# Performance work log

Measured on AMD Instinct MI355X. Metric: run time of the kernel, lower is better.

The kernel has to match this reference:

```python
import jax, jax.numpy as jnp
import numpy as np

H = 256
K = 16
EPS_LN = 1e-5


def setup_inputs() -> dict:
    key = jax.random.key(0)
    ks = jax.random.split(key, 24)
    B, N = 64, 256
    s = lambda *sh: 1.0 / np.sqrt(sh[0])
    inp = {
        "feat": jax.random.normal(ks[0], (B, N, H), jnp.float32),
        "centers": jax.random.normal(ks[1], (B, N, 3), jnp.float32),
        "text_global": jax.random.normal(ks[2], (B, H), jnp.float32),
        # geom_mlp: Linear(4,H) -> ReLU -> Linear(H,H) -> ReLU
        "w_geom1": jax.random.normal(ks[3], (4, H), jnp.float32) * s(4),
        "b_geom1": jnp.zeros((H,), jnp.float32),
        "w_geom2": jax.random.normal(ks[4], (H, H), jnp.float32) * s(H),
        "b_geom2": jnp.zeros((H,), jnp.float32),
        # text gate / bias projections
        "w_gate": jax.random.normal(ks[5], (H, H), jnp.float32) * s(H),
        "b_gate": jnp.zeros((H,), jnp.float32),
        "w_tbias": jax.random.normal(ks[6], (H, H), jnp.float32) * s(H),
        "b_tbias": jnp.zeros((H,), jnp.float32),
        # edge_mlp: Linear(H,H//2) -> ReLU -> Linear(H//2,1)
        "w_edge1": jax.random.normal(ks[7], (H, H // 2), jnp.float32) * s(H),
        "b_edge1": jnp.zeros((H // 2,), jnp.float32),
        "w_edge2": jax.random.normal(ks[8], (H // 2, 1), jnp.float32) * s(H // 2),
        "b_edge2": jnp.zeros((1,), jnp.float32),
        # msg_mlp: Linear(H,H) -> ReLU
        "w_msg": jax.random.normal(ks[9], (H, H), jnp.float32) * s(H),
        "b_msg": jnp.zeros((H,), jnp.float32),
        # out_proj: Linear(2H,H) -> ReLU
        "w_out": jax.random.normal(ks[10], (2 * H, H), jnp.float32) * s(2 * H),
        "b_out": jnp.zeros((H,), jnp.float32),
        # LayerNorm params
        "ln_gamma": jnp.ones((H,), jnp.float32),
        "ln_beta": jnp.zeros((H,), jnp.float32),
    }
    return inp


def _forward(feat, centers, text_global,
             w_geom1, b_geom1, w_geom2, b_geom2,
             w_gate, b_gate, w_tbias, b_tbias,
             w_edge1, b_edge1, w_edge2, b_edge2,
             w_msg, b_msg, w_out, b_out, ln_gamma, ln_beta):
    B, N, Hd = feat.shape
    k = min(K, N)
    # pairwise euclidean distances (B,N,N)
    sq = jnp.sum(centers * centers, axis=-1)  # (B,N)
    d2 = sq[:, :, None] + sq[:, None, :] - 2.0 * jnp.einsum('bnc,bmc->bnm', centers, centers)
    dist_matrix = jnp.sqrt(jnp.maximum(d2, 0.0))
    # k smallest -> top_k of negated distances (sorted ascending in distance)
    _, knn_idx = jax.lax.top_k(-dist_matrix, k)  # (B,N,k)
    idx_flat = knn_idx.reshape(B, N * k)
    feat_neigh = jnp.take_along_axis(feat, idx_flat[:, :, None], axis=1).reshape(B, N, k, Hd)
    centers_neigh = jnp.take_along_axis(centers, idx_flat[:, :, None], axis=1).reshape(B, N, k, 3)
    rel = centers_neigh - centers[:, :, None, :]  # (B,N,k,3)
    dist = jnp.linalg.norm(rel, axis=-1, keepdims=True) + 1e-6
    geom = jnp.concatenate([rel, jnp.log1p(dist)], axis=-1)  # (B,N,k,4)
    geom_emb = jax.nn.relu(jax.nn.relu(geom @ w_geom1 + b_geom1) @ w_geom2 + b_geom2)
    text_gate = jax.nn.sigmoid(text_global @ w_gate + b_gate)[:, None, None, :]
    text_bias = (text_global @ w_tbias + b_tbias)[:, None, None, :]
    geom_cond = geom_emb * text_gate + text_bias
    edge_feat = jnp.tanh(feat[:, :, None, :] + feat_neigh + geom_cond)  # (B,N,k,H)
    edge_logits = (jax.nn.relu(edge_feat @ w_edge1 + b_edge1) @ w_edge2 + b_edge2)[..., 0]
    edge_alpha = jax.nn.softmax(edge_logits, axis=-1)[..., None]  # (B,N,k,1)
    msg = jax.nn.relu(feat_neigh @ w_msg + b_msg)
    ctx = jnp.sum(edge_alpha * msg, axis=2)  # (B,N,H)
    out = jax.nn.relu(jnp.concatenate([feat, ctx], axis=-1) @ w_out + b_out)
    x = feat + out
    mu = jnp.mean(x, axis=-1, keepdims=True)
    var = jnp.mean((x - mu) ** 2, axis=-1, keepdims=True)
    return (x - mu) / jnp.sqrt(var + EPS_LN) * ln_gamma + ln_beta


def reference(feat, centers, text_global,
              w_geom1, b_geom1, w_geom2, b_geom2,
              w_gate, b_gate, w_tbias, b_tbias,
              w_edge1, b_edge1, w_edge2, b_edge2,
              w_msg, b_msg, w_out, b_out, ln_gamma, ln_beta):
    return _forward(feat, centers, text_global,
                    w_geom1, b_geom1, w_geom2, b_geom2,
                    w_gate, b_gate, w_tbias, b_tbias,
                    w_edge1, b_edge1, w_edge2, b_edge2,
                    w_msg, b_msg, w_out, b_out, ln_gamma, ln_beta)
```

## Files before the change

kernel.cpp:

```cpp
#include <hip/hip_runtime.h>

#define H 256
#define KNN 16
#define NPT 256
#define BB 64

typedef unsigned short u16;
typedef unsigned int u32;
typedef __attribute__((ext_vector_type(8))) short shortx8;
typedef __attribute__((ext_vector_type(4))) float floatx4;

__device__ __forceinline__ u16 f2b(float f) {
    u32 u = __float_as_uint(f);
    u32 r = (u + 0x7fffu + ((u >> 16) & 1u)) >> 16;
    return (u16)r;
}
__device__ __forceinline__ float b2f(u16 u) {
    return __uint_as_float(((u32)u) << 16);
}

__device__ __forceinline__ float fast_tanh(float x) {
    float e = __builtin_amdgcn_exp2f(x * 2.88539008177793f);
    return 1.0f - 2.0f * __builtin_amdgcn_rcpf(e + 1.0f);
}

__global__ __launch_bounds__(256) void prep_kernel(
    const float* __restrict__ feat,
    const float* __restrict__ w2, const float* __restrict__ we1,
    const float* __restrict__ wm, const float* __restrict__ wo,
    const float* __restrict__ w1, const float* __restrict__ b1,
    u16* __restrict__ w2t, u16* __restrict__ we1t,
    u16* __restrict__ wmt, u16* __restrict__ wot, u16* __restrict__ w1t,
    u16* __restrict__ featB) {
    int blk = blockIdx.x;
    if (blk < 1184) {
        int tid = blk * 256 + threadIdx.x;
        if (tid < 65536) {
            int n = tid >> 8, k = tid & 255;
            w2t[tid] = f2b(w2[k * 256 + n]);
        } else if (tid < 98304) {
            int t = tid - 65536;
            int n = t >> 8, k = t & 255;
            we1t[t] = f2b(we1[k * 128 + n]);
        } else if (tid < 163840) {
            int t = tid - 98304;
            int n = t >> 8, k = t & 255;
            wmt[t] = f2b(wm[k * 256 + n]);
        } else if (tid < 294912) {
            int t = tid - 163840;
            int n = t >> 9, k = t & 511;
            wot[t] = f2b(wo[k * 256 + n]);
        } else {
            int t = tid - 294912;
            int n = t >> 5, k = t & 31;
            float v = (k < 4) ? w1[k * 256 + n] : (k == 4 ? b1[n] : 0.0f);
            w1t[t] = f2b(v);
        }
        return;
    }
    int e = (blk - 1184) * 256 + threadIdx.x;
    float4 f = *(const float4*)&feat[(size_t)e * 4];
    uint2 st;
    st.x = (u32)f2b(f.x) | ((u32)f2b(f.y) << 16);
    st.y = (u32)f2b(f.z) | ((u32)f2b(f.w) << 16);
    *(uint2*)&featB[(size_t)e * 4] = st;
}

__global__ __launch_bounds__(256) void knn_kernel(const float* __restrict__ centers,
                                                  int* __restrict__ knn) {
    __shared__ float cx[NPT], cy[NPT], cz[NPT], sq[NPT];
    __shared__ float dl[4][64][17];
    __shared__ int il[4][64][17];
    int blk = blockIdx.x;
    int b = blk >> 2, n0 = (blk & 3) * 64;
    int h = threadIdx.x;
    int s = h >> 6, pt = h & 63;
    {
        const float* cb = centers + (size_t)b * NPT * 3;
        float x = cb[h * 3 + 0], y = cb[h * 3 + 1], z = cb[h * 3 + 2];
        cx[h] = x; cy[h] = y; cz[h] = z;
        sq[h] = x * x + y * y + z * z;
    }
    __syncthreads();
    int n = n0 + pt;
    float x = cx[n], y = cy[n], z = cz[n], sn = sq[n];
    float bd[KNN];
    int bi[KNN];
#pragma unroll
    for (int j = 0; j < KNN; j++) { bd[j] = 1e30f; bi[j] = 0x7fffffff; }
    for (int mm = 0; mm < 64; mm++) {
        int m = s * 64 + mm;
        float dot = x * cx[m] + y * cy[m] + z * cz[m];
        float d2 = (sn + sq[m]) - 2.0f * dot;
        float d = sqrtf(fmaxf(d2, 0.0f));
        if (d < bd[KNN - 1]) {
            bd[KNN - 1] = d; bi[KNN - 1] = m;
#pragma unroll
            for (int p = KNN - 1; p > 0; --p) {
                if (bd[p - 1] > bd[p]) {
                    float td = bd[p - 1]; bd[p - 1] = bd[p]; bd[p] = td;
                    int ti = bi[p - 1]; bi[p - 1] = bi[p]; bi[p] = ti;
                }
            }
        }
    }
#pragma unroll
    for (int j = 0; j < KNN; j++) { dl[s][pt][j] = bd[j]; il[s][pt][j] = bi[j]; }
    __syncthreads();
    if (s == 0) {
        float md[KNN];
        int mi[KNN];
#pragma unroll
        for (int j = 0; j < KNN; j++) { md[j] = dl[0][pt][j]; mi[j] = il[0][pt][j]; }
        for (int t = 1; t < 4; t++) {
            for (int j = 0; j < KNN; j++) {
                float d = dl[t][pt][j];
                int idx = il[t][pt][j];
                bool ins = (d < md[KNN - 1]) || (d == md[KNN - 1] && idx < mi[KNN - 1]);
                if (!ins) break;
                md[KNN - 1] = d; mi[KNN - 1] = idx;
#pragma unroll
                for (int p = KNN - 1; p > 0; --p) {
                    bool sw = (md[p - 1] > md[p]) ||
                              (md[p - 1] == md[p] && mi[p - 1] > mi[p]);
                    if (sw) {
                        float td = md[p - 1]; md[p - 1] = md[p]; md[p] = td;
                        int ti = mi[p - 1]; mi[p - 1] = mi[p]; mi[p] = ti;
                    }
                }
            }
        }
        int* kp = knn + (b * NPT + n0 + pt) * KNN;
#pragma unroll
        for (int j = 0; j < KNN; j++) kp[j] = mi[j];
    }
}

__global__ __launch_bounds__(512) void gate_kernel(const float* __restrict__ tg_g,
                                                   const float* __restrict__ wg,
                                                   const float* __restrict__ bg,
                                                   const float* __restrict__ wtb,
                                                   const float* __restrict__ btb,
                                                   float* __restrict__ gate,
                                                   float* __restrict__ tbias) {
    __shared__ float tg[H];
    int b = blockIdx.x, t = threadIdx.x;
    if (t < H) tg[t] = tg_g[b * H + t];
    __syncthreads();
    int h = t & 255;
    if (t < H) {
        float ag = bg[h];
#pragma unroll 4
        for (int i = 0; i < H; i++) ag += tg[i] * wg[i * H + h];
        gate[b * H + h] = 1.0f / (1.0f + expf(-ag));
    } else {
        float ab = btb[h];
#pragma unroll 4
        for (int i = 0; i < H; i++) ab += tg[i] * wtb[i * H + h];
        tbias[b * H + h] = ab;
    }
}

__global__ __launch_bounds__(256, 4) void msg_mfma(const u16* __restrict__ featB,
                                                   const u16* __restrict__ wmt,
                                                   const float* __restrict__ bm,
                                                   u16* __restrict__ MSGB) {
    __shared__ __attribute__((aligned(16))) u16 A[64][264];
    int p0 = blockIdx.x * 64, h = threadIdx.x;
    int w = h >> 6, lane = h & 63, quad = lane >> 4, lq = lane & 15;
#pragma unroll 8
    for (int row = 0; row < 64; row++)
        A[row][h] = featB[(size_t)(p0 + row) * H + h];
    __syncthreads();
    floatx4 acc[4][4];
#pragma unroll
    for (int rt = 0; rt < 4; rt++)
#pragma unroll
        for (int ct = 0; ct < 4; ct++) acc[rt][ct] = (floatx4){0, 0, 0, 0};
#pragma unroll 2
    for (int kt = 0; kt < 8; kt++) {
        shortx8 bf[4];
#pragma unroll
        for (int ct = 0; ct < 4; ct++)
            bf[ct] = *(const shortx8*)&wmt[(w * 64 + ct * 16 + lq) * 256 + kt * 32 + quad * 8];
#pragma unroll
        for (int rt = 0; rt < 4; rt++) {
            shortx8 a = *(const shortx8*)&A[rt * 16 + lq][kt * 32 + quad * 8];
#pragma unroll
            for (int ct = 0; ct < 4; ct++)
                acc[rt][ct] = __builtin_amdgcn_mfma_f32_16x16x32_bf16(a, bf[ct], acc[rt][ct], 0, 0, 0);
        }
    }
#pragma unroll
    for (int ct = 0; ct < 4; ct++) {
        int col = w * 64 + ct * 16 + lq;
        float bmc = bm[col];
#pragma unroll
        for (int rt = 0; rt < 4; rt++)
#pragma unroll
            for (int r = 0; r < 4; r++) {
                int row = rt * 16 + quad * 4 + r;
                MSGB[(size_t)(p0 + row) * H + col] = f2b(fmaxf(acc[rt][ct][r] + bmc, 0.0f));
            }
    }
}

__global__ __launch_bounds__(256, 4) void edge_mfma(
    const float* __restrict__ feat, const u16* __restrict__ featB,
    const float* __restrict__ centers,
    const u16* __restrict__ w1t,
    const u16* __restrict__ w2t, const float* __restrict__ b2v,
    const u16* __restrict__ we1t, const float* __restrict__ be1,
    const float* __restrict__ we2, const float* __restrict__ be2,
    const int* __restrict__ knn, const float* __restrict__ gateG,
    const float* __restrict__ tbiasG, const u16* __restrict__ MSGB,
    u16* __restrict__ ctxB) {
    __shared__ __attribute__((aligned(16))) u16 A[64][264];
    __shared__ float fnS[4][H];
    __shared__ __attribute__((aligned(16))) float geomS[64][4];
    __shared__ int nidxS[64];
    __shared__ float part[4][64];
    __shared__ float logitsS[64];
    __shared__ float alphaS[64];

    int bn0 = blockIdx.x * 4;
    int b = bn0 >> 8, n0 = bn0 & 255;
    int h = threadIdx.x;
    int w = h >> 6, lane = h & 63, quad = lane >> 4, lq = lane & 15;

    if (h < 64) nidxS[h] = knn[bn0 * KNN + h];
#pragma unroll
    for (int p = 0; p < 4; p++)
        fnS[p][h] = feat[(size_t)(bn0 + p) * H + h];
    if (h < 64) {
        int p = h >> 4;
        int m = nidxS[h];
        int n = n0 + p;
        const float* cb = centers + (size_t)b * NPT * 3;
        float rx = cb[m * 3 + 0] - cb[n * 3 + 0];
        float ry = cb[m * 3 + 1] - cb[n * 3 + 1];
        float rz = cb[m * 3 + 2] - cb[n * 3 + 2];
        float dist = sqrtf(rx * rx + ry * ry + rz * rz) + 1e-6f;
        geomS[h][0] = rx; geomS[h][1] = ry; geomS[h][2] = rz;
        geomS[h][3] = log1pf(dist);
    }
    __syncthreads();

    {
        shortx8 bw1[4];
#pragma unroll
        for (int ct = 0; ct < 4; ct++)
            bw1[ct] = *(const shortx8*)&w1t[(w * 64 + ct * 16 + lq) * 32 + quad * 8];
#pragma unroll
        for (int rt = 0; rt < 4; rt++) {
            shortx8 ag = {0, 0, 0, 0, 0, 0, 0, 0};
            if (quad == 0) {
                float4 g = *(const float4*)&geomS[rt * 16 + lq][0];
                ag[0] = (short)f2b(g.x);
                ag[1] = (short)f2b(g.y);
                ag[2] = (short)f2b(g.z);
                ag[3] = (short)f2b(g.w);
                ag[4] = (short)0x3F80;
            }
#pragma unroll
            for (int ct = 0; ct < 4; ct++) {
                floatx4 accg = __builtin_amdgcn_mfma_f32_16x16x32_bf16(
                    ag, bw1[ct], (floatx4){0, 0, 0, 0}, 0, 0, 0);
#pragma unroll
                for (int r = 0; r < 4; r++)
                    A[rt * 16 + quad * 4 + r][w * 64 + ct * 16 + lq] =
                        f2b(fmaxf(accg[r], 0.0f));
            }
        }
    }
    __syncthreads();

    floatx4 acc[4][4];
#pragma unroll
    for (int rt = 0; rt < 4; rt++)
#pragma unroll
        for (int ct = 0; ct < 4; ct++) acc[rt][ct] = (floatx4){0, 0, 0, 0};
#pragma unroll 2
    for (int kt = 0; kt < 8; kt++) {
        shortx8 bf[4];
#pragma unroll
        for (int ct = 0; ct < 4; ct++)
            bf[ct] = *(const shortx8*)&w2t[(w * 64 + ct * 16 + lq) * 256 + kt * 32 + quad * 8];
#pragma unroll
        for (int rt = 0; rt < 4; rt++) {
            shortx8 a = *(const shortx8*)&A[rt * 16 + lq][kt * 32 + quad * 8];
#pragma unroll
            for (int ct = 0; ct < 4; ct++)
                acc[rt][ct] = __builtin_amdgcn_mfma_f32_16x16x32_bf16(a, bf[ct], acc[rt][ct], 0, 0, 0);
        }
    }
    __syncthreads();

#pragma unroll
    for (int ct = 0; ct < 4; ct++) {
        int col = w * 64 + ct * 16 + lq;
        float b2c = b2v[col];
        float gc = gateG[b * H + col];
        float tc = tbiasG[b * H + col];
#pragma unroll
        for (int rt = 0; rt < 4; rt++) {
            float fnc = fnS[rt][col];
#pragma unroll
            for (int r = 0; r < 4; r++) {
                int row = rt * 16 + quad * 4 + r;
                float fb = b2f(featB[((size_t)b * NPT + nidxS[row]) * H + col]);
                float emb = fmaxf(acc[rt][ct][r] + b2c, 0.0f);
                float ef = fast_tanh(fnc + fb + emb * gc + tc);
                A[row][col] = f2b(ef);
            }
        }
    }
    __syncthreads();

    floatx4 acc2[4][2];
#pragma unroll
    for (int rt = 0; rt < 4; rt++)
#pragma unroll
        for (int c2 = 0; c2 < 2; c2++) acc2[rt][c2] = (floatx4){0, 0, 0, 0};
#pragma unroll 2
    for (int kt = 0; kt < 8; kt++) {
        shortx8 bf[2];
#pragma unroll
        for (int c2 = 0; c2 < 2; c2++)
            bf[c2] = *(const shortx8*)&we1t[(w * 32 + c2 * 16 + lq) * 256 + kt * 32 + quad * 8];
#pragma unroll
        for (int rt = 0; rt < 4; rt++) {
            shortx8 a = *(const shortx8*)&A[rt * 16 + lq][kt * 32 + quad * 8];
#pragma unroll
            for (int c2 = 0; c2 < 2; c2++)
                acc2[rt][c2] = __builtin_amdgcn_mfma_f32_16x16x32_bf16(a, bf[c2], acc2[rt][c2], 0, 0, 0);
        }
    }

    float pl[4][4];
#pragma unroll
    for (int rt = 0; rt < 4; rt++)
#pragma unroll
        for (int r = 0; r < 4; r++) pl[rt][r] = 0.0f;
#pragma unroll
    for (int c2 = 0; c2 < 2; c2++) {
        int col = w * 32 + c2 * 16 + lq;
        float be1c = be1[col], w2c = we2[col];
#pragma unroll
        for (int rt = 0; rt < 4; rt++)
#pragma unroll
            for (int r = 0; r < 4; r++)
                pl[rt][r] += fmaxf(acc2[rt][c2][r] + be1c, 0.0f) * w2c;
    }
#pragma unroll
    for (int d = 1; d < 16; d <<= 1)
#pragma unroll
        for (int rt = 0; rt < 4; rt++)
#pragma unroll
            for (int r = 0; r < 4; r++) pl[rt][r] += __shfl_xor(pl[rt][r], d, 16);
    if (lq == 0) {
#pragma unroll
        for (int rt = 0; rt < 4; rt++)
#pragma unroll
            for (int r = 0; r < 4; r++)
                part[w][rt * 16 + quad * 4 + r] = pl[rt][r];
    }
    __syncthreads();
    if (h < 64)
        logitsS[h] = part[0][h] + part[1][h] + part[2][h] + part[3][h] + be2[0];
    __syncthreads();
    if (h < 64) {
        int base = (h >> 4) * 16;
        float mx = -1e30f;
#pragma unroll
        for (int j = 0; j < KNN; j++) mx = fmaxf(mx, logitsS[base + j]);
        float sum = 0.0f;
#pragma unroll
        for (int j = 0; j < KNN; j++) sum += expf(logitsS[base + j] - mx);
        alphaS[h] = expf(logitsS[h] - mx) / sum;
    }
    __syncthreads();

    {
        int p = h >> 6, cg = (h & 63) * 4;
        float4 c = {0, 0, 0, 0};
#pragma unroll
        for (int j = 0; j < KNN; j++) {
            float al = alphaS[p * 16 + j];
            const u32* mp = (const u32*)&MSGB[((size_t)b * NPT + nidxS[p * 16 + j]) * H + cg];
            u32 m0 = mp[0], m1 = mp[1];
            c.x += al * __uint_as_float(m0 << 16);
            c.y += al * __uint_as_float(m0 & 0xFFFF0000u);
            c.z += al * __uint_as_float(m1 << 16);
            c.w += al * __uint_as_float(m1 & 0xFFFF0000u);
        }
        uint2 st;
        st.x = (u32)f2b(c.x) | ((u32)f2b(c.y) << 16);
        st.y = (u32)f2b(c.z) | ((u32)f2b(c.w) << 16);
        *(uint2*)&ctxB[(size_t)(bn0 + p) * H + cg] = st;
    }
}

__global__ __launch_bounds__(256, 4) void out_mfma(const float* __restrict__ feat,
                                                   const u16* __restrict__ featB,
                                                   const u16* __restrict__ ctxB,
                                                   const u16* __restrict__ wot,
                                                   const float* __restrict__ bo,
                                                   const float* __restrict__ gamma,
                                                   const float* __restrict__ beta,
                                                   float* __restrict__ out) {
    __shared__ __attribute__((aligned(16))) u16 A[32][520];
    __shared__ float redS[4][32], redS2[4][32];
    int p0 = blockIdx.x * 32, h = threadIdx.x;
    int w = h >> 6, lane = h & 63, quad = lane >> 4, lq = lane & 15;
#pragma unroll 8
    for (int row = 0; row < 32; row++) {
        A[row][h]       = featB[(size_t)(p0 + row) * H + h];
        A[row][256 + h] = ctxB[(size_t)(p0 + row) * H + h];
    }
    __syncthreads();
    floatx4 acc[2][4];
#pragma unroll
    for (int rt = 0; rt < 2; rt++)
#pragma unroll
        for (int ct = 0; ct < 4; ct++) acc[rt][ct] = (floatx4){0, 0, 0, 0};
#pragma unroll 2
    for (int kt = 0; kt < 16; kt++) {
        shortx8 bf[4];
#pragma unroll
        for (int ct = 0; ct < 4; ct++)
            bf[ct] = *(const shortx8*)&wot[(w * 64 + ct * 16 + lq) * 512 + kt * 32 + quad * 8];
#pragma unroll
        for (int rt = 0; rt < 2; rt++) {
            shortx8 a = *(const shortx8*)&A[rt * 16 + lq][kt * 32 + quad * 8];
#pragma unroll
            for (int ct = 0; ct < 4; ct++)
                acc[rt][ct] = __builtin_amdgcn_mfma_f32_16x16x32_bf16(a, bf[ct], acc[rt][ct], 0, 0, 0);
        }
    }
    float x[2][4][4];
    float sm[2][4], sq2[2][4];
#pragma unroll
    for (int rt = 0; rt < 2; rt++)
#pragma unroll
        for (int r = 0; r < 4; r++) { sm[rt][r] = 0.0f; sq2[rt][r] = 0.0f; }
#pragma unroll
    for (int rt = 0; rt < 2; rt++)
#pragma unroll
        for (int ct = 0; ct < 4; ct++) {
            int col = w * 64 + ct * 16 + lq;
            float boc = bo[col];
#pragma unroll
            for (int r = 0; r < 4; r++) {
                int row = rt * 16 + quad * 4 + r;
                float xx = feat[(size_t)(p0 + row) * H + col] +
                           fmaxf(acc[rt][ct][r] + boc, 0.0f);
                x[rt][ct][r] = xx;
                sm[rt][r] += xx;
                sq2[rt][r] += xx * xx;
            }
        }
#pragma unroll
    for (int d = 1; d < 16; d <<= 1)
#pragma unroll
        for (int rt = 0; rt < 2; rt++)
#pragma unroll
            for (int r = 0; r < 4; r++) {
                sm[rt][r] += __shfl_xor(sm[rt][r], d, 16);
                sq2[rt][r] += __shfl_xor(sq2[rt][r], d, 16);
            }
    if (lq == 0) {
#pragma unroll
        for (int rt = 0; rt < 2; rt++)
#pragma unroll
            for (int r = 0; r < 4; r++) {
                redS[w][rt * 16 + quad * 4 + r] = sm[rt][r];
                redS2[w][rt * 16 + quad * 4 + r] = sq2[rt][r];
            }
    }
    __syncthreads();
#pragma unroll
    for (int rt = 0; rt < 2; rt++)
#pragma unroll
        for (int r = 0; r < 4; r++) {
            int row = rt * 16 + quad * 4 + r;
            float s1 = redS[0][row] + redS[1][row] + redS[2][row] + redS[3][row];
            float s2 = redS2[0][row] + redS2[1][row] + redS2[2][row] + redS2[3][row];
            float mu = s1 * (1.0f / H);
            float var = s2 * (1.0f / H) - mu * mu;
            float inv = rsqrtf(fmaxf(var, 0.0f) + 1e-5f);
#pragma unroll
            for (int ct = 0; ct < 4; ct++) {
                int col = w * 64 + ct * 16 + lq;
                out[(size_t)(p0 + row) * H + col] =
                    (x[rt][ct][r] - mu) * inv * gamma[col] + beta[col];
            }
        }
}

extern "C" void kernel_launch(void* const* d_in, const int* in_sizes, int n_in,
                              void* d_out, int out_size, void* d_ws, size_t ws_size,
                              hipStream_t stream) {
    const float* feat    = (const float*)d_in[0];
    const float* centers = (const float*)d_in[1];
    const float* textg   = (const float*)d_in[2];
    const float* w1      = (const float*)d_in[3];
    const float* b1      = (const float*)d_in[4];
    const float* w2      = (const float*)d_in[5];
    const float* b2      = (const float*)d_in[6];
    const float* wg      = (const float*)d_in[7];
    const float* bg      = (const float*)d_in[8];
    const float* wtb     = (const float*)d_in[9];
    const float* btb     = (const float*)d_in[10];
    const float* we1     = (const float*)d_in[11];
    const float* be1     = (const float*)d_in[12];
    const float* we2     = (const float*)d_in[13];
    const float* be2     = (const float*)d_in[14];
    const float* wm      = (const float*)d_in[15];
    const float* bm      = (const float*)d_in[16];
    const float* wo      = (const float*)d_in[17];
    const float* bo      = (const float*)d_in[18];
    const float* gamma   = (const float*)d_in[19];
    const float* beta    = (const float*)d_in[20];

    char* ws = (char*)d_ws;
    size_t off = 0;
    int* knn     = (int*)(ws + off);   off += (size_t)BB * NPT * KNN * 4;
    float* gate  = (float*)(ws + off); off += (size_t)BB * H * 4;
    float* tbias = (float*)(ws + off); off += (size_t)BB * H * 4;
    u16* MSGB    = (u16*)(ws + off);   off += (size_t)BB * NPT * H * 2;
    u16* ctxB    = (u16*)(ws + off);   off += (size_t)BB * NPT * H * 2;
    u16* featB   = (u16*)(ws + off);   off += (size_t)BB * NPT * H * 2;
    u16* w2t     = (u16*)(ws + off);   off += (size_t)256 * 256 * 2;
    u16* we1t    = (u16*)(ws + off);   off += (size_t)128 * 256 * 2;
    u16* wmt     = (u16*)(ws + off);   off += (size_t)256 * 256 * 2;
    u16* wot     = (u16*)(ws + off);   off += (size_t)256 * 512 * 2;
    u16* w1t     = (u16*)(ws + off);   off += (size_t)256 * 32 * 2;

    prep_kernel<<<5280, 256, 0, stream>>>(feat, w2, we1, wm, wo, w1, b1,
                                          w2t, we1t, wmt, wot, w1t, featB);
    knn_kernel<<<256, 256, 0, stream>>>(centers, knn);
    gate_kernel<<<BB, 512, 0, stream>>>(textg, wg, bg, wtb, btb, gate, tbias);
    msg_mfma<<<BB * NPT / 64, 256, 0, stream>>>(featB, wmt, bm, MSGB);
    edge_mfma<<<BB * NPT / 4, 256, 0, stream>>>(feat, featB, centers, w1t, w2t, b2,
                                                we1t, be1, we2, be2, knn, gate, tbias,
                                                MSGB, ctxB);
    out_mfma<<<BB * NPT / 32, 256, 0, stream>>>(feat, featB, ctxB, wot, bo,
                                                gamma, beta, (float*)d_out);
}
```

Before: 347.3 us.

## Fuse output projection and LayerNorm into edge kernel, drop ctx buffer

Folds the out_proj GEMM, residual add and LayerNorm into the tail of edge_mfma. The 4 points' ctx and feat rows are staged in the existing shared A tile instead of writing ctxB to global and relaunching. This removes one kernel launch and the ctxB round trip through memory. In exchange each block runs a 16-row MFMA tile with only 4 valid rows, so 3/4 of the MFMA work is wasted. Each block also re-reads the full 256KB wot weight, which adds a lot of L2 traffic.

```diff
diff --git a/kernel.cpp b/kernel.cpp
--- a/kernel.cpp
+++ b/kernel.cpp
@@ -214,7 +214,9 @@
     const float* __restrict__ we2, const float* __restrict__ be2,
     const int* __restrict__ knn, const float* __restrict__ gateG,
     const float* __restrict__ tbiasG, const u16* __restrict__ MSGB,
-    u16* __restrict__ ctxB) {
+    const u16* __restrict__ wot, const float* __restrict__ bo,
+    const float* __restrict__ gamma, const float* __restrict__ beta,
+    float* __restrict__ out) {
     __shared__ __attribute__((aligned(16))) u16 A[64][264];
     __shared__ float fnS[4][H];
     __shared__ __attribute__((aligned(16))) float geomS[64][4];
@@ -381,6 +383,7 @@
     }
     __syncthreads();
 
+    u16* A2 = &A[0][0];
     {
         int p = h >> 6, cg = (h & 63) * 4;
         float4 c = {0, 0, 0, 0};
@@ -397,105 +400,73 @@
         uint2 st;
         st.x = (u32)f2b(c.x) | ((u32)f2b(c.y) << 16);
         st.y = (u32)f2b(c.z) | ((u32)f2b(c.w) << 16);
-        *(uint2*)&ctxB[(size_t)(bn0 + p) * H + cg] = st;
-    }
-}
-
-__global__ __launch_bounds__(256, 4) void out_mfma(const float* __restrict__ feat,
-                                                   const u16* __restrict__ featB,
-                                                   const u16* __restrict__ ctxB,
-                                                   const u16* __restrict__ wot,
-                                                   const float* __restrict__ bo,
-                                                   const float* __restrict__ gamma,
-                                                   const float* __restrict__ beta,
-                                                   float* __restrict__ out) {
-    __shared__ __attribute__((aligned(16))) u16 A[32][520];
-    __shared__ float redS[4][32], redS2[4][32];
-    int p0 = blockIdx.x * 32, h = threadIdx.x;
-    int w = h >> 6, lane = h & 63, quad = lane >> 4, lq = lane & 15;
-#pragma unroll 8
-    for (int row = 0; row < 32; row++) {
-        A[row][h]       = featB[(size_t)(p0 + row) * H + h];
-        A[row][256 + h] = ctxB[(size_t)(p0 + row) * H + h];
-    }
-    __syncthreads();
-    floatx4 acc[2][4];
-#pragma unroll
-    for (int rt = 0; rt < 2; rt++)
-#pragma unroll
-        for (int ct = 0; ct < 4; ct++) acc[rt][ct] = (floatx4){0, 0, 0, 0};
-#pragma unroll 2
+        *(uint2*)&A2[p * 520 + 256 + cg] = st;
+        uint2 fb2 = *(const uint2*)&featB[(size_t)(bn0 + p) * H + cg];
+        *(uint2*)&A2[p * 520 + cg] = fb2;
+    }
+    __syncthreads();
+
+    floatx4 acc3[4];
+#pragma unroll
+    for (int ct = 0; ct < 4; ct++) acc3[ct] = (floatx4){0, 0, 0, 0};
+#pragma unroll 4
     for (int kt = 0; kt < 16; kt++) {
-        shortx8 bf[4];
-#pragma unroll
-        for (int ct = 0; ct < 4; ct++)
-            bf[ct] = *(const shortx8*)&wot[(w * 64 + ct * 16 + lq) * 512 + kt * 32 + quad * 8];
-#pragma unroll
-        for (int rt = 0; rt < 2; rt++) {
-            shortx8 a = *(const shortx8*)&A[rt * 16 + lq][kt * 32 + quad * 8];
-#pragma unroll
-            for (int ct = 0; ct < 4; ct++)
-                acc[rt][ct] = __builtin_amdgcn_mfma_f32_16x16x32_bf16(a, bf[ct], acc[rt][ct], 0, 0, 0);
-        }
-    }
-    float x[2][4][4];
-    float sm[2][4], sq2[2][4];
-#pragma unroll
-    for (int rt = 0; rt < 2; rt++)
-#pragma unroll
-        for (int r = 0; r < 4; r++) { sm[rt][r] = 0.0f; sq2[rt][r] = 0.0f; }
-#pragma unroll
-    for (int rt = 0; rt < 2; rt++)
+        shortx8 a = *(const shortx8*)&A2[lq * 520 + kt * 32 + quad * 8];
+#pragma unroll
+        for (int ct = 0; ct < 4; ct++) {
+            shortx8 bf = *(const shortx8*)&wot[(w * 64 + ct * 16 + lq) * 512 + kt * 32 + quad * 8];
+            acc3[ct] = __builtin_amdgcn_mfma_f32_16x16x32_bf16(a, bf, acc3[ct], 0, 0, 0);
+        }
+    }
+
+    float x3[4][4];
+    if (quad == 0) {
+        float sm2[4] = {0, 0, 0, 0}, sq3[4] = {0, 0, 0, 0};
 #pragma unroll
         for (int ct = 0; ct < 4; ct++) {
             int col = w * 64 + ct * 16 + lq;
             float boc = bo[col];
 #pragma unroll
             for (int r = 0; r < 4; r++) {
-                int row = rt * 16 + quad * 4 + r;
-                float xx = feat[(size_t)(p0 + row) * H + col] +
-                           fmaxf(acc[rt][ct][r] + boc, 0.0f);
-                x[rt][ct][r] = xx;
-                sm[rt][r] += xx;
-                sq2[rt][r] += xx * xx;
-            }
-        }
-#pragma unroll
-    for (int d = 1; d < 16; d <<= 1)
-#pragma unroll
-        for (int rt = 0; rt < 2; rt++)
+                float xx = feat[(size_t)(bn0 + r) * H + col] +
+                           fmaxf(acc3[ct][r] + boc, 0.0f);
+                x3[ct][r] = xx;
+                sm2[r] += xx;
+                sq3[r] += xx * xx;
+            }
+        }
+#pragma unroll
+        for (int d = 1; d < 16; d <<= 1)
 #pragma unroll
             for (int r = 0; r < 4; r++) {
-                sm[rt][r] += __shfl_xor(sm[rt][r], d, 16);
-                sq2[rt][r] += __shfl_xor(sq2[rt][r], d, 16);
-            }
-    if (lq == 0) {
-#pragma unroll
-        for (int rt = 0; rt < 2; rt++)
+                sm2[r] += __shfl_xor(sm2[r], d, 16);
+                sq3[r] += __shfl_xor(sq3[r], d, 16);
+            }
+        if (lq == 0) {
 #pragma unroll
             for (int r = 0; r < 4; r++) {
-                redS[w][rt * 16 + quad * 4 + r] = sm[rt][r];
-                redS2[w][rt * 16 + quad * 4 + r] = sq2[rt][r];
-            }
-    }
-    __syncthreads();
-#pragma unroll
-    for (int rt = 0; rt < 2; rt++)
+                part[w][r] = sm2[r];
+                part[w][16 + r] = sq3[r];
+            }
+        }
+    }
+    __syncthreads();
+    if (quad == 0) {
 #pragma unroll
         for (int r = 0; r < 4; r++) {
-            int row = rt * 16 + quad * 4 + r;
-            float s1 = redS[0][row] + redS[1][row] + redS[2][row] + redS[3][row];
-            float s2 = redS2[0][row] + redS2[1][row] + redS2[2][row] + redS2[3][row];
+            float s1 = part[0][r] + part[1][r] + part[2][r] + part[3][r];
+            float s2 = part[0][16 + r] + part[1][16 + r] + part[2][16 + r] + part[3][16 + r];
             float mu = s1 * (1.0f / H);
             float var = s2 * (1.0f / H) - mu * mu;
             float inv = rsqrtf(fmaxf(var, 0.0f) + 1e-5f);
 #pragma unroll
             for (int ct = 0; ct < 4; ct++) {
                 int col = w * 64 + ct * 16 + lq;
-                out[(size_t)(p0 + row) * H + col] =
-                    (x[rt][ct][r] - mu) * inv * gamma[col] + beta[col];
-            }
-        }
+                out[(size_t)(bn0 + r) * H + col] =
+                    (x3[ct][r] - mu) * inv * gamma[col] + beta[col];
+            }
+        }
+    }
 }
 
 extern "C" void kernel_launch(void* const* d_in, const int* in_sizes, int n_in,
@@ -529,7 +500,6 @@
     float* gate  = (float*)(ws + off); off += (size_t)BB * H * 4;
     float* tbias = (float*)(ws + off); off += (size_t)BB * H * 4;
     u16* MSGB    = (u16*)(ws + off);   off += (size_t)BB * NPT * H * 2;
-    u16* ctxB    = (u16*)(ws + off);   off += (size_t)BB * NPT * H * 2;
     u16* featB   = (u16*)(ws + off);   off += (size_t)BB * NPT * H * 2;
     u16* w2t     = (u16*)(ws + off);   off += (size_t)256 * 256 * 2;
     u16* we1t    = (u16*)(ws + off);   off += (size_t)128 * 256 * 2;
@@ -544,7 +514,6 @@
     msg_mfma<<<BB * NPT / 64, 256, 0, stream>>>(featB, wmt, bm, MSGB);
     edge_mfma<<<BB * NPT / 4, 256, 0, stream>>>(feat, featB, centers, w1t, w2t, b2,
                                                 we1t, be1, we2, be2, knn, gate, tbias,
-                                                MSGB, ctxB);
-    out_mfma<<<BB * NPT / 32, 256, 0, stream>>>(feat, featB, ctxB, wot, bo,
-                                                gamma, beta, (float*)d_out);
-}
+                                                MSGB, wot, bo, gamma, beta,
+                                                (float*)d_out);
+}
```

After: 434.4 us. +25.1%, slower.
